# Optimization experiments

Measured on AMD Instinct MI355X. Metric: run time of the kernel, lower is better.

Reference implementation:

```python
import jax, jax.numpy as jnp
import numpy as np

D_MODEL = 1024
HEADS = 16
D_K = D_MODEL // HEADS  # 64


def setup_inputs() -> dict:
    key = jax.random.key(0)
    ks = jax.random.split(key, 9)
    B, S = 4, 2048
    values = jax.random.normal(ks[0], (B, S, D_MODEL), dtype=jnp.float32)
    keys = jax.random.normal(ks[1], (B, S, D_MODEL), dtype=jnp.float32)
    query = jax.random.normal(ks[2], (B, S, D_MODEL), dtype=jnp.float32)
    mask = jax.random.randint(ks[3], (1, 1, S, S), 0, 2, dtype=jnp.int32)
    # per-head projection weights (shared across heads), torch Linear layout (out, in)
    sc = 1.0 / np.sqrt(D_K)
    Wv = jax.random.uniform(ks[4], (D_K, D_K), jnp.float32, -sc, sc)
    Wk = jax.random.uniform(ks[5], (D_K, D_K), jnp.float32, -sc, sc)
    Wq = jax.random.uniform(ks[6], (D_K, D_K), jnp.float32, -sc, sc)
    so = 1.0 / np.sqrt(D_MODEL)
    Wo = jax.random.uniform(ks[7], (D_MODEL, D_MODEL), jnp.float32, -so, so)
    bo = jax.random.uniform(ks[8], (D_MODEL,), jnp.float32, -so, so)
    return {"values": values, "keys": keys, "query": query, "mask": mask,
            "Wv": Wv, "Wk": Wk, "Wq": Wq, "Wo": Wo, "bo": bo}


def reference(values, keys, query, mask, Wv, Wk, Wq, Wo, bo):
    n, q_len, d = query.shape
    v_len, k_len = values.shape[1], keys.shape[1]
    # reshape to (n, len, heads, d_k) and apply shared per-head linear (x @ W^T)
    v = values.reshape(n, v_len, HEADS, D_K) @ Wv.T
    k = keys.reshape(n, k_len, HEADS, D_K) @ Wk.T
    q = query.reshape(n, q_len, HEADS, D_K) @ Wq.T
    # scores: (n, h, q, k)
    scores = jnp.einsum('nqhd,nkhd->nhqk', q, k)
    scores = jnp.where(mask == 0, jnp.float32(-1e20), scores)
    attn = jax.nn.softmax(scores / jnp.sqrt(jnp.float32(D_K)), axis=3)
    out = jnp.einsum('nhqk,nkhd->nqhd', attn, v).reshape(n, q_len, HEADS * D_K)
    return out @ Wo.T + bo
```

## Files before the change

kernel.cpp:

```cpp
#include <hip/hip_runtime.h>

#define B 4
#define S 2048
#define H 16
#define DK 64
#define DM 1024
#define NTILES (S / 64)
#define QSCALE 0.18033688011112042f

typedef _Float16 half_t;
typedef __attribute__((ext_vector_type(8))) _Float16 half8v;
typedef __attribute__((ext_vector_type(2))) _Float16 half2v;
typedef __attribute__((ext_vector_type(2))) __fp16   fp16x2;
typedef __attribute__((ext_vector_type(4))) float    float4v;

__device__ __forceinline__ unsigned pkh(float lo, float hi) {
    union { fp16x2 h; unsigned u; } cvt;
    cvt.h = __builtin_amdgcn_cvt_pkrtz(lo, hi);
    return cvt.u;
}
__device__ __forceinline__ float fast_exp2(float x) {
#if __has_builtin(__builtin_amdgcn_exp2f)
    return __builtin_amdgcn_exp2f(x);
#else
    return __expf(x * 0.69314718055994531f);
#endif
}
__device__ __forceinline__ half8v cvt8h(float4 a, float4 b) {
    half8v r;
    r[0] = (half_t)a.x; r[1] = (half_t)a.y; r[2] = (half_t)a.z; r[3] = (half_t)a.w;
    r[4] = (half_t)b.x; r[5] = (half_t)b.y; r[6] = (half_t)b.z; r[7] = (half_t)b.w;
    return r;
}
__device__ __forceinline__ void gl2lds16(const void* g, void* l) {
    __builtin_amdgcn_global_load_lds(
        (const __attribute__((address_space(1))) unsigned int*)g,
        (__attribute__((address_space(3))) unsigned int*)l, 16, 0, 0);
}

__global__ __launch_bounds__(256) void mask_pack_kernel(
    const int* __restrict__ mask, unsigned long long* __restrict__ mp)
{
    int t = blockIdx.x * 256 + threadIdx.x;
    int m = mask[t];
    unsigned long long b = __ballot(m != 0);
    if ((threadIdx.x & 63) == 0) mp[t >> 6] = b;
}

__global__ __launch_bounds__(256) void wcvt_kernel(
    const float* __restrict__ Wo, half_t* __restrict__ Wh)
{
    int t = (blockIdx.x * 256 + threadIdx.x) * 4;
    float4 wv = *(const float4*)(Wo + t);
    union { half_t h[4]; uint2 u; } cvt;
    cvt.h[0] = (half_t)wv.x; cvt.h[1] = (half_t)wv.y;
    cvt.h[2] = (half_t)wv.z; cvt.h[3] = (half_t)wv.w;
    *(uint2*)(Wh + t) = cvt.u;
}

__global__ __launch_bounds__(256) void qkv_proj_kernel(
    const float* __restrict__ xv, const float* __restrict__ xk, const float* __restrict__ xq,
    const float* __restrict__ Wv, const float* __restrict__ Wk, const float* __restrict__ Wq,
    half_t* __restrict__ vtw, half_t* __restrict__ kw, half_t* __restrict__ qw)
{
    const int y = blockIdx.y;
    const float* x; const float* W;
    if (y == 0)      { x = xv; W = Wv; }
    else if (y == 1) { x = xk; W = Wk; }
    else             { x = xq; W = Wq; }

    const int tid = threadIdx.x;
    const int w = tid >> 6, L = tid & 63, a = L & 15, g = L >> 4;
    const int bx  = blockIdx.x;
    const int st  = bx & 31;
    const int bh  = bx >> 5;
    const int b_  = bh >> 4, h = bh & 15;
    const int s0b = st * 64;

    half8v wF[4][2];
    #pragma unroll
    for (int t = 0; t < 4; ++t)
        #pragma unroll
        for (int c = 0; c < 2; ++c) {
            const float* wr = W + (size_t)(16 * t + a) * 64 + 32 * c + 8 * g;
            wF[t][c] = cvt8h(*(const float4*)wr, *(const float4*)(wr + 4));
        }

    const float* xr = x + ((size_t)(b_ * S) + s0b + 16 * w + a) * DM + h * 64 + 8 * g;
    half8v xF0 = cvt8h(*(const float4*)(xr),      *(const float4*)(xr + 4));
    half8v xF1 = cvt8h(*(const float4*)(xr + 32), *(const float4*)(xr + 36));

    const float4v z4 = {0.0f, 0.0f, 0.0f, 0.0f};

    if (y == 0) {
        const int c   = 16 * w + a;
        const int pos = 32 * (c >> 5) + 8 * ((c >> 2) & 3) + 4 * ((c >> 4) & 1) + (c & 3);
        #pragma unroll
        for (int mt = 0; mt < 4; ++mt) {
            float4v D = __builtin_amdgcn_mfma_f32_16x16x32_f16(wF[mt][0], xF0, z4, 0, 0, 0);
            D = __builtin_amdgcn_mfma_f32_16x16x32_f16(wF[mt][1], xF1, D, 0, 0, 0);
            #pragma unroll
            for (int r = 0; r < 4; ++r)
                vtw[((size_t)bh * 64 + 16 * mt + 4 * g + r) * S + s0b + pos] = (half_t)D[r];
        }
    } else {
        half_t* out = (y == 1) ? kw : qw;
        const float scale = (y == 2) ? QSCALE : 1.0f;
        #pragma unroll
        for (int nt = 0; nt < 4; ++nt) {
            float4v D = __builtin_amdgcn_mfma_f32_16x16x32_f16(xF0, wF[nt][0], z4, 0, 0, 0);
            D = __builtin_amdgcn_mfma_f32_16x16x32_f16(xF1, wF[nt][1], D, 0, 0, 0);
            #pragma unroll
            for (int r = 0; r < 4; ++r)
                out[((size_t)bh * S + s0b + 16 * w + 4 * g + r) * 64 + 16 * nt + a] =
                    (half_t)(D[r] * scale);
        }
    }
}

__global__ __launch_bounds__(256, 4) void flash_attn_kernel(
    const half_t* __restrict__ q, const half_t* __restrict__ k,
    const half_t* __restrict__ vt, const unsigned long long* __restrict__ mp,
    half_t* __restrict__ att)
{
    __shared__ half_t KV[2][2][64 * 64];

    const int tid = threadIdx.x;
    const int w   = tid >> 6;
    const int L   = tid & 63;
    const int a   = L & 15;
    const int g   = L >> 4;
    const int bh  = blockIdx.x;
    const int b_  = bh >> 4, h = bh & 15;
    const int qs  = blockIdx.y * 128 + w * 32;

    const half_t* qb = q  + (size_t)bh * S * 64;
    const half_t* kb = k  + (size_t)bh * S * 64;
    const half_t* vb = vt + (size_t)bh * 64 * S;

    half8v qB[2][2];
    #pragma unroll
    for (int gq = 0; gq < 2; ++gq) {
        const half_t* qr = qb + (size_t)(qs + 16 * gq + a) * 64;
        qB[gq][0] = *(const half8v*)(qr +      g * 8);
        qB[gq][1] = *(const half8v*)(qr + 32 + g * 8);
    }

    const unsigned long long* mr0 = mp + (size_t)(qs      + a) * NTILES;
    const unsigned long long* mr1 = mp + (size_t)(qs + 16 + a) * NTILES;

    int srow[2], schk[2];
    #pragma unroll
    for (int i = 0; i < 2; ++i) {
        int p   = (w * 2 + i) * 64 + L;
        srow[i] = p >> 3;
        schk[i] = (p & 7) ^ (srow[i] & 7);
    }

    half8v ones;
    #pragma unroll
    for (int i = 0; i < 8; ++i) ones[i] = (half_t)1.0f;

    const float4v z4 = {0.0f, 0.0f, 0.0f, 0.0f};
    float4v o[2][4] = {{z4, z4, z4, z4}, {z4, z4, z4, z4}};
    float4v lD[2] = {z4, z4};

    #pragma unroll
    for (int i = 0; i < 2; ++i) {
        gl2lds16(kb + (size_t)srow[i] * 64 + schk[i] * 8, &KV[0][0][(w * 2 + i) * 64 * 8]);
        gl2lds16(vb + (size_t)srow[i] * S + schk[i] * 8,  &KV[0][1][(w * 2 + i) * 64 * 8]);
    }

    for (int kt = 0; kt < NTILES; ++kt) {
        const int cur = kt & 1;
        __syncthreads();

        if (kt + 1 < NTILES) {
            const int nk = kt + 1;
            #pragma unroll
            for (int i = 0; i < 2; ++i) {
                gl2lds16(kb + ((size_t)(nk * 64 + srow[i])) * 64 + schk[i] * 8,
                         &KV[cur ^ 1][0][(w * 2 + i) * 64 * 8]);
                gl2lds16(vb + (size_t)srow[i] * S + nk * 64 + schk[i] * 8,
                         &KV[cur ^ 1][1][(w * 2 + i) * 64 * 8]);
            }
        }

        const unsigned long long mw0 = mr0[kt];
        const unsigned long long mw1 = mr1[kt];

        const half_t* Kb = &KV[cur][0][0];
        const half_t* Vb = &KV[cur][1][0];

        half8v kB[4][2], vA[4][2];
        #pragma unroll
        for (int nt = 0; nt < 4; ++nt)
            #pragma unroll
            for (int c = 0; c < 2; ++c) {
                const int off = ((16 * nt + a) * 8 + ((4 * c + g) ^ (a & 7))) * 8;
                kB[nt][c] = *(const half8v*)(Kb + off);
                vA[nt][c] = *(const half8v*)(Vb + off);
            }

        #pragma unroll
        for (int gq = 0; gq < 2; ++gq) {
            float4v st[4];
            #pragma unroll
            for (int nt = 0; nt < 4; ++nt) {
                st[nt] = __builtin_amdgcn_mfma_f32_16x16x32_f16(kB[nt][0], qB[gq][0], z4, 0, 0, 0);
                st[nt] = __builtin_amdgcn_mfma_f32_16x16x32_f16(kB[nt][1], qB[gq][1], st[nt], 0, 0, 0);
            }

            const unsigned long long mw = gq ? mw1 : mw0;
            float e[4][4];
            #pragma unroll
            for (int nt = 0; nt < 4; ++nt) {
                unsigned bnt = (unsigned)(mw >> (16 * nt + 4 * g));
                #pragma unroll
                for (int r = 0; r < 4; ++r) {
                    float ee = fast_exp2(st[nt][r]);
                    e[nt][r] = ((bnt >> r) & 1u) ? ee : 0.0f;
                }
            }

            half8v pB[2];
            #pragma unroll
            for (int c = 0; c < 2; ++c) {
                union { unsigned u[4]; half8v hv; } cvt;
                cvt.u[0] = pkh(e[2*c  ][0], e[2*c  ][1]);
                cvt.u[1] = pkh(e[2*c  ][2], e[2*c  ][3]);
                cvt.u[2] = pkh(e[2*c+1][0], e[2*c+1][1]);
                cvt.u[3] = pkh(e[2*c+1][2], e[2*c+1][3]);
                pB[c] = cvt.hv;
            }

            #pragma unroll
            for (int nt = 0; nt < 4; ++nt) {
                o[gq][nt] = __builtin_amdgcn_mfma_f32_16x16x32_f16(vA[nt][0], pB[0], o[gq][nt], 0, 0, 0);
                o[gq][nt] = __builtin_amdgcn_mfma_f32_16x16x32_f16(vA[nt][1], pB[1], o[gq][nt], 0, 0, 0);
            }
            lD[gq] = __builtin_amdgcn_mfma_f32_16x16x32_f16(ones, pB[0], lD[gq], 0, 0, 0);
            lD[gq] = __builtin_amdgcn_mfma_f32_16x16x32_f16(ones, pB[1], lD[gq], 0, 0, 0);
        }
    }

    #pragma unroll
    for (int gq = 0; gq < 2; ++gq) {
        const float inv = 1.0f / lD[gq][0];
        const size_t row = (size_t)(b_ * S + qs + 16 * gq + a);
        #pragma unroll
        for (int nt = 0; nt < 4; ++nt) {
            union { unsigned u[2]; uint2 u2; } cvt;
            cvt.u[0] = pkh(o[gq][nt][0] * inv, o[gq][nt][1] * inv);
            cvt.u[1] = pkh(o[gq][nt][2] * inv, o[gq][nt][3] * inv);
            *(uint2*)(att + row * DM + h * 64 + 16 * nt + 4 * g) = cvt.u2;
        }
    }
}

__global__ __launch_bounds__(256, 2) void out_proj_kernel(
    const half_t* __restrict__ X, const half_t* __restrict__ Wh,
    const float* __restrict__ bo, float* __restrict__ out)
{
    __shared__ half_t SA[2][128 * 64], SB[2][128 * 64];

    const int tid = threadIdx.x;
    const int w = tid >> 6, L = tid & 63, a = L & 15, g = L >> 4;
    const int wm = w >> 1, wn = w & 1;
    const int r0 = blockIdx.x * 128;
    const int n0 = blockIdx.y * 128;

    int prow[4], pchk[4], pbase[4];
    #pragma unroll
    for (int i = 0; i < 4; ++i) {
        int p    = w * 256 + i * 64 + L;
        prow[i]  = p >> 3;
        pchk[i]  = (p & 7) ^ (prow[i] & 7);
        pbase[i] = (w * 256 + i * 64) * 8;
    }

    const float4v z4 = {0.0f, 0.0f, 0.0f, 0.0f};
    float4v acc[4][4];
    #pragma unroll
    for (int mt = 0; mt < 4; ++mt)
        #pragma unroll
        for (int nt = 0; nt < 4; ++nt) acc[mt][nt] = z4;

    #pragma unroll
    for (int i = 0; i < 4; ++i) {
        gl2lds16(X  + (size_t)(r0 + prow[i]) * DM + pchk[i] * 8, &SA[0][pbase[i]]);
        gl2lds16(Wh + (size_t)(n0 + prow[i]) * DM + pchk[i] * 8, &SB[0][pbase[i]]);
    }

    for (int kt = 0; kt < DM / 64; ++kt) {
        const int cur = kt & 1;
        __syncthreads();

        if (kt + 1 < DM / 64) {
            const int k0 = (kt + 1) * 64;
            #pragma unroll
            for (int i = 0; i < 4; ++i) {
                gl2lds16(X  + (size_t)(r0 + prow[i]) * DM + k0 + pchk[i] * 8, &SA[cur ^ 1][pbase[i]]);
                gl2lds16(Wh + (size_t)(n0 + prow[i]) * DM + k0 + pchk[i] * 8, &SB[cur ^ 1][pbase[i]]);
            }
        }

        half8v bF[4][2];
        #pragma unroll
        for (int nt = 0; nt < 4; ++nt)
            #pragma unroll
            for (int c = 0; c < 2; ++c) {
                const int rb  = 64 * wn + 16 * nt + a;
                const int off = (rb * 8 + ((4 * c + g) ^ (rb & 7))) * 8;
                bF[nt][c] = *(const half8v*)&SB[cur][off];
            }

        #pragma unroll
        for (int mt = 0; mt < 4; ++mt) {
            const int ra   = 64 * wm + 16 * mt + a;
            const int off0 = (ra * 8 + ((0 + g) ^ (ra & 7))) * 8;
            const int off1 = (ra * 8 + ((4 + g) ^ (ra & 7))) * 8;
            half8v a0 = *(const half8v*)&SA[cur][off0];
            half8v a1 = *(const half8v*)&SA[cur][off1];
            #pragma unroll
            for (int nt = 0; nt < 4; ++nt) {
                float4v acv = acc[mt][nt];
                acv = __builtin_amdgcn_mfma_f32_16x16x32_f16(a0, bF[nt][0], acv, 0, 0, 0);
                acv = __builtin_amdgcn_mfma_f32_16x16x32_f16(a1, bF[nt][1], acv, 0, 0, 0);
                acc[mt][nt] = acv;
            }
        }
    }

    #pragma unroll
    for (int mt = 0; mt < 4; ++mt) {
        const int m0 = r0 + 64 * wm + 16 * mt + 4 * g;
        #pragma unroll
        for (int nt = 0; nt < 4; ++nt) {
            const int n = n0 + 64 * wn + 16 * nt + a;
            const float bias = bo[n];
            #pragma unroll
            for (int r = 0; r < 4; ++r)
                out[(size_t)(m0 + r) * DM + n] = acc[mt][nt][r] + bias;
        }
    }
}

extern "C" void kernel_launch(void* const* d_in, const int* in_sizes, int n_in,
                              void* d_out, int out_size, void* d_ws, size_t ws_size,
                              hipStream_t stream) {
    (void)in_sizes; (void)n_in; (void)out_size; (void)ws_size;
    const float* values = (const float*)d_in[0];
    const float* keys   = (const float*)d_in[1];
    const float* query  = (const float*)d_in[2];
    const int*   mask   = (const int*)d_in[3];
    const float* Wv     = (const float*)d_in[4];
    const float* Wk     = (const float*)d_in[5];
    const float* Wq     = (const float*)d_in[6];
    const float* Wo     = (const float*)d_in[7];
    const float* bo     = (const float*)d_in[8];
    float* out = (float*)d_out;

    const size_t per = (size_t)B * H * S * DK;
    half_t* qw  = (half_t*)d_ws;
    half_t* kw  = qw + per;
    half_t* vtw = kw + per;
    unsigned long long* mp = (unsigned long long*)(vtw + per);
    half_t* atth = (half_t*)(mp + (size_t)S * S / 64);
    half_t* woh  = atth + per;

    mask_pack_kernel<<<S * S / 256, 256, 0, stream>>>(mask, mp);
    wcvt_kernel<<<DM * DM / 1024, 256, 0, stream>>>(Wo, woh);

    dim3 g1(B * H * (S / 64), 3);
    qkv_proj_kernel<<<g1, 256, 0, stream>>>(values, keys, query, Wv, Wk, Wq, vtw, kw, qw);

    dim3 g2(B * H, S / 128);
    flash_attn_kernel<<<g2, 256, 0, stream>>>(qw, kw, vtw, mp, atth);

    dim3 g3(B * S / 128, DM / 128);
    out_proj_kernel<<<g3, 256, 0, stream>>>(atth, woh, bo, out);
}
```

Baseline: 357.1 us.

## Double query rows per flash-attention wave and fuse mask-pack with weight conversion

Each wave in the flash attention kernel now handles 64 query rows instead of 32, so a block covers 256 rows and every K/V tile staged in LDS is reused across twice as many queries. This halves global K/V traffic and LDS loads per query, at the cost of more registers per thread. The launch-bounds occupancy hint is dropped and the grid shrinks to 512 blocks, which may lower occupancy and make it harder to hide latency. Separately, the mask packing and Wo fp16 conversion kernels are merged into one launch to save a kernel launch.

After: 328.1 us. 8.1% less time.

```diff
diff --git a/kernel.cpp b/kernel.cpp
--- a/kernel.cpp
+++ b/kernel.cpp
@@ -10,7 +10,6 @@
 
 typedef _Float16 half_t;
 typedef __attribute__((ext_vector_type(8))) _Float16 half8v;
-typedef __attribute__((ext_vector_type(2))) _Float16 half2v;
 typedef __attribute__((ext_vector_type(2))) __fp16   fp16x2;
 typedef __attribute__((ext_vector_type(4))) float    float4v;
 
@@ -38,24 +37,25 @@
         (__attribute__((address_space(3))) unsigned int*)l, 16, 0, 0);
 }
 
-__global__ __launch_bounds__(256) void mask_pack_kernel(
-    const int* __restrict__ mask, unsigned long long* __restrict__ mp)
-{
-    int t = blockIdx.x * 256 + threadIdx.x;
-    int m = mask[t];
-    unsigned long long b = __ballot(m != 0);
-    if ((threadIdx.x & 63) == 0) mp[t >> 6] = b;
-}
-
-__global__ __launch_bounds__(256) void wcvt_kernel(
+#define MASK_BLOCKS (S * S / 256)
+__global__ __launch_bounds__(256) void prep_kernel(
+    const int* __restrict__ mask, unsigned long long* __restrict__ mp,
     const float* __restrict__ Wo, half_t* __restrict__ Wh)
 {
-    int t = (blockIdx.x * 256 + threadIdx.x) * 4;
-    float4 wv = *(const float4*)(Wo + t);
-    union { half_t h[4]; uint2 u; } cvt;
-    cvt.h[0] = (half_t)wv.x; cvt.h[1] = (half_t)wv.y;
-    cvt.h[2] = (half_t)wv.z; cvt.h[3] = (half_t)wv.w;
-    *(uint2*)(Wh + t) = cvt.u;
+    int bx = blockIdx.x;
+    if (bx < MASK_BLOCKS) {
+        int t = bx * 256 + threadIdx.x;
+        int m = mask[t];
+        unsigned long long b = __ballot(m != 0);
+        if ((threadIdx.x & 63) == 0) mp[t >> 6] = b;
+    } else {
+        int t = ((bx - MASK_BLOCKS) * 256 + threadIdx.x) * 4;
+        float4 wv = *(const float4*)(Wo + t);
+        union { half_t h[4]; uint2 u; } cvt;
+        cvt.h[0] = (half_t)wv.x; cvt.h[1] = (half_t)wv.y;
+        cvt.h[2] = (half_t)wv.z; cvt.h[3] = (half_t)wv.w;
+        *(uint2*)(Wh + t) = cvt.u;
+    }
 }
 
 __global__ __launch_bounds__(256) void qkv_proj_kernel(
@@ -118,7 +118,7 @@
     }
 }
 
-__global__ __launch_bounds__(256, 4) void flash_attn_kernel(
+__global__ __launch_bounds__(256) void flash_attn_kernel(
     const half_t* __restrict__ q, const half_t* __restrict__ k,
     const half_t* __restrict__ vt, const unsigned long long* __restrict__ mp,
     half_t* __restrict__ att)
@@ -132,22 +132,24 @@
     const int g   = L >> 4;
     const int bh  = blockIdx.x;
     const int b_  = bh >> 4, h = bh & 15;
-    const int qs  = blockIdx.y * 128 + w * 32;
+    const int qs  = blockIdx.y * 256 + w * 64;
 
     const half_t* qb = q  + (size_t)bh * S * 64;
     const half_t* kb = k  + (size_t)bh * S * 64;
     const half_t* vb = vt + (size_t)bh * 64 * S;
 
-    half8v qB[2][2];
-    #pragma unroll
-    for (int gq = 0; gq < 2; ++gq) {
+    half8v qB[4][2];
+    #pragma unroll
+    for (int gq = 0; gq < 4; ++gq) {
         const half_t* qr = qb + (size_t)(qs + 16 * gq + a) * 64;
         qB[gq][0] = *(const half8v*)(qr +      g * 8);
         qB[gq][1] = *(const half8v*)(qr + 32 + g * 8);
     }
 
-    const unsigned long long* mr0 = mp + (size_t)(qs      + a) * NTILES;
-    const unsigned long long* mr1 = mp + (size_t)(qs + 16 + a) * NTILES;
+    const unsigned long long* mr[4];
+    #pragma unroll
+    for (int gq = 0; gq < 4; ++gq)
+        mr[gq] = mp + (size_t)(qs + 16 * gq + a) * NTILES;
 
     int srow[2], schk[2];
     #pragma unroll
@@ -162,8 +164,12 @@
     for (int i = 0; i < 8; ++i) ones[i] = (half_t)1.0f;
 
     const float4v z4 = {0.0f, 0.0f, 0.0f, 0.0f};
-    float4v o[2][4] = {{z4, z4, z4, z4}, {z4, z4, z4, z4}};
-    float4v lD[2] = {z4, z4};
+    float4v o[4][4];
+    #pragma unroll
+    for (int gq = 0; gq < 4; ++gq)
+        #pragma unroll
+        for (int nt = 0; nt < 4; ++nt) o[gq][nt] = z4;
+    float4v lD[4] = {z4, z4, z4, z4};
 
     #pragma unroll
     for (int i = 0; i < 2; ++i) {
@@ -186,8 +192,9 @@
             }
         }
 
-        const unsigned long long mw0 = mr0[kt];
-        const unsigned long long mw1 = mr1[kt];
+        unsigned long long mw[4];
+        #pragma unroll
+        for (int gq = 0; gq < 4; ++gq) mw[gq] = mr[gq][kt];
 
         const half_t* Kb = &KV[cur][0][0];
         const half_t* Vb = &KV[cur][1][0];
@@ -203,7 +210,7 @@
             }
 
         #pragma unroll
-        for (int gq = 0; gq < 2; ++gq) {
+        for (int gq = 0; gq < 4; ++gq) {
             float4v st[4];
             #pragma unroll
             for (int nt = 0; nt < 4; ++nt) {
@@ -211,11 +218,10 @@
                 st[nt] = __builtin_amdgcn_mfma_f32_16x16x32_f16(kB[nt][1], qB[gq][1], st[nt], 0, 0, 0);
             }
 
-            const unsigned long long mw = gq ? mw1 : mw0;
             float e[4][4];
             #pragma unroll
             for (int nt = 0; nt < 4; ++nt) {
-                unsigned bnt = (unsigned)(mw >> (16 * nt + 4 * g));
+                unsigned bnt = (unsigned)(mw[gq] >> (16 * nt + 4 * g));
                 #pragma unroll
                 for (int r = 0; r < 4; ++r) {
                     float ee = fast_exp2(st[nt][r]);
@@ -245,7 +251,7 @@
     }
 
     #pragma unroll
-    for (int gq = 0; gq < 2; ++gq) {
+    for (int gq = 0; gq < 4; ++gq) {
         const float inv = 1.0f / lD[gq][0];
         const size_t row = (size_t)(b_ * S + qs + 16 * gq + a);
         #pragma unroll
@@ -369,13 +375,12 @@
     half_t* atth = (half_t*)(mp + (size_t)S * S / 64);
     half_t* woh  = atth + per;
 
-    mask_pack_kernel<<<S * S / 256, 256, 0, stream>>>(mask, mp);
-    wcvt_kernel<<<DM * DM / 1024, 256, 0, stream>>>(Wo, woh);
+    prep_kernel<<<MASK_BLOCKS + DM * DM / 1024, 256, 0, stream>>>(mask, mp, Wo, woh);
 
     dim3 g1(B * H * (S / 64), 3);
     qkv_proj_kernel<<<g1, 256, 0, stream>>>(values, keys, query, Wv, Wk, Wq, vtw, kw, qw);
 
-    dim3 g2(B * H, S / 128);
+    dim3 g2(B * H, S / 256);
     flash_attn_kernel<<<g2, 256, 0, stream>>>(qw, kw, vtw, mp, atth);
 
     dim3 g3(B * S / 128, DM / 128);
```
